# Kernel tuning notes

Measured on AMD Instinct MI355X. Metric: run time of the kernel, lower is better.

## Reference

```python
import jax, jax.numpy as jnp
import numpy as np
import math

B, T, C, NH, NLQ, NLKV, DHR = 2, 1024, 2048, 16, 512, 512, 64
HS = C // NH


def _rope(x, cos, sin):
    # x: [B,T,H,D]; cos/sin: [T,D//2]. Rotates pairs (even,odd) like torch apply_rotary_emb.
    xr = x.reshape(x.shape[:-1] + (-1, 2))
    re, im = xr[..., 0], xr[..., 1]
    c = cos[None, :, None, :]
    s = sin[None, :, None, :]
    out = jnp.stack([re * c - im * s, re * s + im * c], axis=-1)
    return out.reshape(x.shape)


def setup_inputs() -> dict:
    key = jax.random.key(0)
    ks = jax.random.split(key, 9)
    sc = jnp.float32(0.02)
    x = jax.random.normal(ks[0], (B, T, C), jnp.float32)
    W_dq = jax.random.normal(ks[1], (NLQ, C), jnp.float32) * sc
    W_uq = jax.random.normal(ks[2], (C, NLQ), jnp.float32) * sc
    W_dkv = jax.random.normal(ks[3], (NLKV, C), jnp.float32) * sc
    W_uk = jax.random.normal(ks[4], (C, NLKV), jnp.float32) * sc
    W_uv = jax.random.normal(ks[5], (C, NLKV), jnp.float32) * sc
    W_qr = jax.random.normal(ks[6], (NH * DHR, NLQ), jnp.float32) * sc
    W_kr = jax.random.normal(ks[7], (DHR, C), jnp.float32) * sc
    W_o = jax.random.normal(ks[8], (C, C), jnp.float32) * sc
    inv = 1.0 / (10000.0 ** (np.arange(0, DHR, 2, dtype=np.float64) / DHR))
    fr = np.outer(np.arange(T), inv)
    freqs_cos = jnp.asarray(np.cos(fr), jnp.float32)
    freqs_sin = jnp.asarray(np.sin(fr), jnp.float32)
    return {"x": x, "freqs_cos": freqs_cos, "freqs_sin": freqs_sin,
            "W_dq": W_dq, "W_uq": W_uq, "W_dkv": W_dkv, "W_uk": W_uk,
            "W_uv": W_uv, "W_qr": W_qr, "W_kr": W_kr, "W_o": W_o}


def reference(x, freqs_cos, freqs_sin, W_dq, W_uq, W_dkv, W_uk, W_uv, W_qr, W_kr, W_o):
    # Training path of FullMHLA (no kv_cache, dropout=0).
    # Absorbed matrices: same memory reinterpretation as torch .view on [out,in] weights.
    k_eff = jnp.einsum('qhd,hdk->hqk', W_uq.reshape(NLQ, NH, HS), W_uk.reshape(NH, HS, NLKV))  # [nh,nlq,nlkv]
    v_eff = (W_uv.T @ W_o.T).reshape(NLKV, NH, HS)  # used as [nlkv,nh,hs]

    c_q = x @ W_dq.T            # [B,T,nlq]
    c_kv = x @ W_dkv.T          # [B,T,nlkv]

    # content scores: c_q @ k_eff @ c_kv^T
    q_abs = jnp.einsum('btq,hqk->bhtk', c_q, k_eff)          # [B,nh,T,nlkv]
    attn_c = jnp.einsum('bhtk,bsk->bhts', q_abs, c_kv)       # [B,nh,T,T]

    # decoupled RoPE scores
    c_kr = x @ W_kr.T                                         # [B,T,dhr]
    k_r = _rope(c_kr[:, :, None, :], freqs_cos, freqs_sin)[:, :, 0, :]   # [B,T,dhr]
    c_qr = (c_q @ W_qr.T).reshape(B, T, NH, DHR)
    q_r = _rope(c_qr, freqs_cos, freqs_sin)                   # [B,T,nh,dhr]
    attn_r = jnp.einsum('bthd,bsd->bhts', q_r, k_r)           # [B,nh,T,T]

    attn = (attn_c + attn_r) / math.sqrt(HS + DHR)
    mask = jnp.triu(jnp.ones((T, T), dtype=bool), k=1)
    attn = jnp.where(mask[None, None], jnp.float32(-jnp.inf), attn)
    attn = jax.nn.softmax(attn, axis=-1)

    # y = attn @ c_kv @ v_eff
    lat = jnp.einsum('bhts,bsk->bhtk', attn, c_kv)            # [B,nh,T,nlkv]
    y = jnp.einsum('bhtk,khd->bthd', lat, v_eff)              # [B,T,nh,hs]
    return y.reshape(B, T, C)
```

## Files before the change

### kernel.cpp

```cpp
#include <hip/hip_runtime.h>

#define Bv   2
#define Tv   1024
#define Cv   2048
#define NHv  16

typedef unsigned short u16;
typedef __attribute__((ext_vector_type(8))) short bf8_t;
typedef __attribute__((ext_vector_type(4))) float f4_t;
typedef __attribute__((ext_vector_type(4))) unsigned short u16x4;
typedef __attribute__((ext_vector_type(8))) unsigned short u16x8;

__device__ __forceinline__ u16 f2bf(float f) {
  union { float f; unsigned u; } v; v.f = f;
  unsigned r = v.u + 0x7fffu + ((v.u >> 16) & 1u);
  return (u16)(r >> 16);
}
__device__ __forceinline__ float bf2f(u16 b) {
  return __uint_as_float((unsigned)b << 16);
}
__device__ __forceinline__ void glds16(const u16* gp, u16* lp) {
  __builtin_amdgcn_global_load_lds(
      (const __attribute__((address_space(1))) void*)gp,
      (__attribute__((address_space(3))) void*)lp, 16, 0, 0);
}

struct Job {
  const u16* A; const u16* B; void* C;
  long sA1, sA2, sB1, sB2, sC1, sC2;
  int K, lda, ldb, ldc, Nact, zdiv, ntx, nty, out_bf;
};
struct JobPack3 { Job j[3]; int cum[4]; };

__global__ __launch_bounds__(256) void gemm_multi(JobPack3 P) {
  const int bid = blockIdx.x;
  const int ji = (bid >= P.cum[1] ? 1 : 0) + (bid >= P.cum[2] ? 1 : 0);
  const Job& J = P.j[ji];
  int local = bid - P.cum[ji];
  const int x = local % J.ntx;
  int rest = local / J.ntx;
  const int y = rest % J.nty;
  const int z = rest / J.nty;
  const int m0 = y * 128, n0 = x * 128;

  const int z1 = z / J.zdiv, z2 = z % J.zdiv;
  const u16* A = J.A + z1 * J.sA1 + z2 * J.sA2;
  const u16* B = J.B + z1 * J.sB1 + z2 * J.sB2;
  const int K = J.K, lda = J.lda, ldb = J.ldb, ldc = J.ldc, Nact = J.Nact;

  __shared__ u16 SMEM[16384];
  u16* As = SMEM;
  u16* Bs = SMEM + 8192;

  const int tid = threadIdx.x, w = tid >> 6, ln = tid & 63;
  const int my = w >> 1, mx = w & 1;
  const int g = ln >> 4, m = ln & 15;

  f4_t acc[4][4];
#pragma unroll
  for (int i = 0; i < 4; ++i)
#pragma unroll
    for (int j = 0; j < 4; ++j) acc[i][j] = (f4_t)0.f;

  for (int k0 = 0; k0 < K; k0 += 64) {
#pragma unroll
    for (int q = 0; q < 4; ++q) {
      int r = 32 * w + 8 * q + (ln >> 3);
      int c = ((ln & 7) - r) & 7;
      glds16(&A[(long)(m0 + r) * lda + k0 + c * 8], &As[(32 * w + 8 * q) * 64]);
      glds16(&B[(long)(n0 + r) * ldb + k0 + c * 8], &Bs[(32 * w + 8 * q) * 64]);
    }
    __syncthreads();
#pragma unroll
    for (int kh = 0; kh < 2; ++kh) {
      bf8_t af[4], bg[4];
#pragma unroll
      for (int mt = 0; mt < 4; ++mt) {
        int row = my * 64 + mt * 16 + m;
        af[mt] = *(const bf8_t*)&As[row * 64 + (((kh * 4 + g) + row) & 7) * 8];
      }
#pragma unroll
      for (int nt = 0; nt < 4; ++nt) {
        int row = mx * 64 + nt * 16 + m;
        bg[nt] = *(const bf8_t*)&Bs[row * 64 + (((kh * 4 + g) + row) & 7) * 8];
      }
#pragma unroll
      for (int mt = 0; mt < 4; ++mt)
#pragma unroll
        for (int nt = 0; nt < 4; ++nt)
          acc[mt][nt] = __builtin_amdgcn_mfma_f32_16x16x32_bf16(
              af[mt], bg[nt], acc[mt][nt], 0, 0, 0);
    }
    __syncthreads();
  }

  if (J.out_bf) {
    u16* Es = SMEM + w * 4096;
#pragma unroll
    for (int mt = 0; mt < 4; ++mt)
#pragma unroll
      for (int nt = 0; nt < 4; ++nt)
#pragma unroll
        for (int r = 0; r < 4; ++r) {
          int row = mt * 16 + g * 4 + r;
          int col = nt * 16 + m;
          Es[row * 64 + (((col >> 3) + row) & 7) * 8 + (col & 7)] =
              f2bf(acc[mt][nt][r]);
        }
    __syncthreads();
    u16* C = (u16*)J.C + z1 * J.sC1 + z2 * J.sC2;
    const long rowbase = (long)(m0 + my * 64 + ln) * ldc + n0 + mx * 64;
#pragma unroll
    for (int c = 0; c < 8; ++c) {
      if (n0 + mx * 64 + c * 8 < Nact) {
        u16x8 v = *(const u16x8*)&Es[ln * 64 + ((c + ln) & 7) * 8];
        *(u16x8*)&C[rowbase + c * 8] = v;
      }
    }
  } else {
    float* C = (float*)J.C + z1 * J.sC1 + z2 * J.sC2;
#pragma unroll
    for (int mt = 0; mt < 4; ++mt)
#pragma unroll
      for (int nt = 0; nt < 4; ++nt)
#pragma unroll
        for (int r = 0; r < 4; ++r) {
          int row = m0 + my * 64 + mt * 16 + g * 4 + r;
          int col = n0 + mx * 64 + nt * 16 + m;
          if (col < Nact) C[(long)row * ldc + col] = acc[mt][nt][r];
        }
  }
}

__global__ __launch_bounds__(256, 3) void attn_part(
    const u16* __restrict__ Qcat,
    const u16* __restrict__ Kcat,
    const u16* __restrict__ ZT,
    float* __restrict__ Opart,
    float* __restrict__ ml,
    float* __restrict__ out) {
  const int x = blockIdx.x;
  const int bh = x & 31, item = x >> 5;
  const int b = bh >> 4, h = bh & 15;
  static const int qtab[40] = {2,3,4,5,6,6,7,7,8,8,9,9,10,10,10,11,11,11,
                               12,12,12,13,13,13,14,14,14,14,15,15,15,15,
                               0,1,4,5,8,9,12,13};
  static const int ctab[40] = {0,0,0,0,0,1,0,1,0,1,0,1,0,1,2,0,1,2,
                               0,1,2,0,1,2,0,1,2,3,0,1,2,3,
                               0,0,1,1,2,2,3,3};
  const int qt = qtab[item], ch = ctab[item];
  const int ns = (qt >> 1) + 1;
  const int s0t = 2 * ch, s1t = min(2 * ch + 2, ns);
  const bool full = (ch == 0) && (qt <= 3);

  __shared__ u16 As[4096];
  __shared__ u16 Bs[8192];
  __shared__ u16 Ps[8192];

  const int tid = threadIdx.x, w = tid >> 6, ln = tid & 63;
  const int g = ln >> 4, m = ln & 15;

  const u16* Qb = Qcat + (long)bh * 589824 + (long)qt * 64 * 576;
  const u16* Kb = Kcat + (long)b * 589824;
  const u16* Zb = ZT + (long)bh * 131072;

  f4_t O[8];
#pragma unroll
  for (int j = 0; j < 8; ++j) O[j] = (f4_t)0.f;
  float mrow[4], lrow[4];
#pragma unroll
  for (int r = 0; r < 4; ++r) { mrow[r] = -3e38f; lrow[r] = 0.f; }

  const float scale = 0.07216878364870322f;

  for (int st = s0t; st < s1t; ++st) {
    f4_t S[8];
#pragma unroll
    for (int j = 0; j < 8; ++j) S[j] = (f4_t)0.f;

    for (int k0 = 0; k0 < 576; k0 += 64) {
#pragma unroll
      for (int q = 0; q < 2; ++q) {
        int r = 16 * w + 8 * q + (ln >> 3);
        int c = ((ln & 7) - r) & 7;
        glds16(&Qb[(long)r * 576 + k0 + c * 8], &As[(16 * w + 8 * q) * 64]);
      }
#pragma unroll
      for (int q = 0; q < 4; ++q) {
        int r = 32 * w + 8 * q + (ln >> 3);
        int c = ((ln & 7) - r) & 7;
        glds16(&Kb[(long)(st * 128 + r) * 576 + k0 + c * 8],
               &Bs[(32 * w + 8 * q) * 64]);
      }
      __syncthreads();
#pragma unroll
      for (int kh = 0; kh < 2; ++kh) {
        int qrow = 16 * w + m;
        bf8_t af = *(const bf8_t*)&As[qrow * 64 + (((kh * 4 + g) + qrow) & 7) * 8];
#pragma unroll
        for (int nt = 0; nt < 8; ++nt) {
          int row = nt * 16 + m;
          bf8_t bb = *(const bf8_t*)&Bs[row * 64 + (((kh * 4 + g) + row) & 7) * 8];
          S[nt] = __builtin_amdgcn_mfma_f32_16x16x32_bf16(af, bb, S[nt], 0, 0, 0);
        }
      }
      __syncthreads();
    }

    const bool diag = (st == (qt >> 1));
#pragma unroll
    for (int nt = 0; nt < 8; ++nt)
#pragma unroll
      for (int r = 0; r < 4; ++r) {
        float v = S[nt][r] * scale;
        if (diag &&
            (st * 128 + nt * 16 + m) > (qt * 64 + 16 * w + g * 4 + r))
          v = -3e38f;
        S[nt][r] = v;
      }

#pragma unroll
    for (int r = 0; r < 4; ++r) {
      float mx = S[0][r];
#pragma unroll
      for (int nt = 1; nt < 8; ++nt) mx = fmaxf(mx, S[nt][r]);
#pragma unroll
      for (int o = 1; o < 16; o <<= 1) mx = fmaxf(mx, __shfl_xor(mx, o, 64));
      float mn = fmaxf(mrow[r], mx);
      float al = __expf(mrow[r] - mn);
      mrow[r] = mn;
      float rs = 0.f;
#pragma unroll
      for (int nt = 0; nt < 8; ++nt) {
        float p = __expf(S[nt][r] - mn);
        S[nt][r] = p;
        rs += p;
      }
#pragma unroll
      for (int o = 1; o < 16; o <<= 1) rs += __shfl_xor(rs, o, 64);
      lrow[r] = lrow[r] * al + rs;
#pragma unroll
      for (int nt = 0; nt < 8; ++nt) O[nt][r] *= al;
    }

#pragma unroll
    for (int nt = 0; nt < 8; ++nt) {
      int colc = nt * 2 + (m >> 3), cole = m & 7;
#pragma unroll
      for (int r = 0; r < 4; ++r) {
        int row = 16 * w + g * 4 + r;
        Ps[row * 128 + ((colc + row) & 15) * 8 + cole] = f2bf(S[nt][r]);
      }
    }

#pragma unroll
    for (int kb = 0; kb < 2; ++kb) {
      __syncthreads();
#pragma unroll
      for (int q = 0; q < 4; ++q) {
        int r = 32 * w + 8 * q + (ln >> 3);
        int c = ((ln & 7) - r) & 7;
        glds16(&Zb[(long)r * 1024 + st * 128 + kb * 64 + c * 8],
               &Bs[(32 * w + 8 * q) * 64]);
      }
      __syncthreads();
#pragma unroll
      for (int kh = 0; kh < 2; ++kh) {
        int qrow = 16 * w + m;
        int chk = kb * 8 + kh * 4 + g;
        bf8_t af = *(const bf8_t*)&Ps[qrow * 128 + ((chk + qrow) & 15) * 8];
#pragma unroll
        for (int nt = 0; nt < 8; ++nt) {
          int row = nt * 16 + m;
          bf8_t bb = *(const bf8_t*)&Bs[row * 64 + (((kh * 4 + g) + row) & 7) * 8];
          O[nt] = __builtin_amdgcn_mfma_f32_16x16x32_bf16(af, bb, O[nt], 0, 0, 0);
        }
      }
    }
    __syncthreads();
  }

  if (full) {
    float* ob = out + ((long)b * Tv + qt * 64 + 16 * w) * 2048 + h * 128;
#pragma unroll
    for (int r = 0; r < 4; ++r) {
      float inv = 1.0f / lrow[r];
#pragma unroll
      for (int nt = 0; nt < 8; ++nt)
        ob[(long)(g * 4 + r) * 2048 + nt * 16 + m] = O[nt][r] * inv;
    }
  } else {
    float* Ob = Opart + (long)x * 8192;
#pragma unroll
    for (int r = 0; r < 4; ++r) {
      int row = 16 * w + g * 4 + r;
#pragma unroll
      for (int nt = 0; nt < 8; ++nt)
        Ob[(long)row * 128 + nt * 16 + m] = O[nt][r];
      if (m == 0) {
        ml[(long)x * 128 + row] = mrow[r];
        ml[(long)x * 128 + 64 + row] = lrow[r];
      }
    }
  }
}

__global__ __launch_bounds__(256) void attn_merge(
    const float* __restrict__ Opart, const float* __restrict__ ml,
    float* __restrict__ out) {
  const int i = blockIdx.x;
  const int rg = i & 3;
  const int combo = i >> 2;
  const int bh = combo & 31, qt = 4 + (combo >> 5);
  const int b = bh >> 4, h = bh & 15;
  static const int NCH[16] = {1,1,1,1,2,2,2,2,3,3,3,3,4,4,4,4};
  static const int ITEM[64] = {
      32,0,0,0,  33,0,0,0,  0,0,0,0,   1,0,0,0,
      2,34,0,0,  3,35,0,0,  4,5,0,0,   6,7,0,0,
      8,9,36,0,  10,11,37,0, 12,13,14,0, 15,16,17,0,
      18,19,20,38, 21,22,23,39, 24,25,26,27, 28,29,30,31};
  const int nch = NCH[qt];
  const int r = threadIdx.x >> 5, c4 = threadIdx.x & 31;
  float* ob = out + ((long)b * Tv + qt * 64 + rg * 16) * 2048 + h * 128;
#pragma unroll
  for (int rr = 0; rr < 2; ++rr) {
    const int lrow = r + rr * 8;
    const int row = rg * 16 + lrow;
    float M = -3e38f, mi[4], li[4];
    for (int k = 0; k < nch; ++k) {
      long p = (long)ITEM[qt * 4 + k] * 32 + bh;
      mi[k] = ml[p * 128 + row];
      li[k] = ml[p * 128 + 64 + row];
      M = fmaxf(M, mi[k]);
    }
    float L = 0.f;
    float ax = 0.f, ay = 0.f, az = 0.f, aw = 0.f;
    for (int k = 0; k < nch; ++k) {
      long p = (long)ITEM[qt * 4 + k] * 32 + bh;
      float e = __expf(mi[k] - M);
      L += li[k] * e;
      float4 v = *(const float4*)&Opart[p * 8192 + (long)row * 128 + c4 * 4];
      ax += v.x * e; ay += v.y * e; az += v.z * e; aw += v.w * e;
    }
    const float inv = 1.0f / L;
    float4 o4 = {ax * inv, ay * inv, az * inv, aw * inv};
    *(float4*)&ob[(long)lrow * 2048 + c4 * 4] = o4;
  }
}

struct CastArgs {
  const float* src[6];
  u16* dst[6];
  long cum[7];
  const float* wkr;
  u16* w3;
};
__global__ void cast_all(CastArgs a, long total4) {
  long i = (long)blockIdx.x * 256 + threadIdx.x;
  if (i < total4) {
    int seg = 0;
    while (i >= a.cum[seg + 1]) ++seg;
    long j = i - a.cum[seg];
    float4 vv = ((const float4*)a.src[seg])[j];
    u16x4 o;
    o[0] = f2bf(vv.x); o[1] = f2bf(vv.y); o[2] = f2bf(vv.z); o[3] = f2bf(vv.w);
    ((u16x4*)a.dst[seg])[j] = o;
  } else {
    long j = i - total4;
    u16x4* W4 = (u16x4*)a.w3;
    if (j < 32768) {
      float4 vv = ((const float4*)a.wkr)[j];
      u16x4 o;
      o[0] = f2bf(vv.x); o[1] = f2bf(vv.y); o[2] = f2bf(vv.z); o[3] = f2bf(vv.w);
      W4[557056 + j] = o;
    } else if (j < 65536) {
      W4[262144 + (j - 32768)] = (u16x4)0;
    } else {
      W4[589824 + (j - 65536)] = (u16x4)0;
    }
  }
}

__global__ __launch_bounds__(256) void tcast2(const float* __restrict__ s0,
                                              u16* __restrict__ d0,
                                              const float* __restrict__ s1,
                                              u16* __restrict__ d1) {
  const float* in = blockIdx.z ? s1 : s0;
  u16* out = blockIdx.z ? d1 : d0;
  __shared__ u16 t[32][33];
  int c0 = blockIdx.x * 32, r0 = blockIdx.y * 32;
  int tx = threadIdx.x & 31, ty = threadIdx.x >> 5;
  for (int i = ty; i < 32; i += 8)
    t[i][tx] = f2bf(in[(long)(r0 + i) * 512 + c0 + tx]);
  __syncthreads();
  for (int i = ty; i < 32; i += 8)
    out[(long)(c0 + i) * 2048 + r0 + tx] = t[tx][i];
}

__global__ void rope_fused(u16* __restrict__ Kcat, const u16* __restrict__ cqr,
                           u16* __restrict__ Qcat,
                           const float* __restrict__ cosf,
                           const float* __restrict__ sinf) {
  int idx = blockIdx.x * 256 + threadIdx.x;
  if (idx < 65536) {
    int i = idx & 31, t = (idx >> 5) & 1023, b = idx >> 15;
    float c = cosf[t * 32 + i], s = sinf[t * 32 + i];
    u16* p = Kcat + ((long)(b * Tv + t) * 576 + 512 + 2 * i);
    float re = bf2f(p[0]), im = bf2f(p[1]);
    p[0] = f2bf(re * c - im * s);
    p[1] = f2bf(re * s + im * c);
  } else {
    int j = idx - 65536;
    int i = j & 31, h = (j >> 5) & 15, t = (j >> 9) & 1023, b = j >> 19;
    float c = cosf[t * 32 + i], s = sinf[t * 32 + i];
    const u16* src = cqr + ((long)(b * Tv + t) * 1024 + h * 64 + 2 * i);
    float re = bf2f(src[0]), im = bf2f(src[1]);
    u16* dst = Qcat + (((long)(b * NHv + h) * Tv + t) * 576 + 512 + 2 * i);
    dst[0] = f2bf(re * c - im * s);
    dst[1] = f2bf(re * s + im * c);
  }
}

__global__ void vred(const float* __restrict__ P, u16* __restrict__ veffT) {
  int i = blockIdx.x * 256 + threadIdx.x;
  float4 v0 = ((const float4*)P)[i];
  float4 v1 = ((const float4*)P)[262144 + i];
  float4 v2 = ((const float4*)P)[524288 + i];
  float4 v3 = ((const float4*)P)[786432 + i];
  u16x4 o;
  o[0] = f2bf(v0.x + v1.x + v2.x + v3.x);
  o[1] = f2bf(v0.y + v1.y + v2.y + v3.y);
  o[2] = f2bf(v0.z + v1.z + v2.z + v3.z);
  o[3] = f2bf(v0.w + v1.w + v2.w + v3.w);
  ((u16x4*)veffT)[i] = o;
}

extern "C" void kernel_launch(void* const* d_in, const int* in_sizes, int n_in,
                              void* d_out, int out_size, void* d_ws,
                              size_t ws_size, hipStream_t stream) {
  const float* x    = (const float*)d_in[0];
  const float* fcos = (const float*)d_in[1];
  const float* fsin = (const float*)d_in[2];
  const float* Wdq  = (const float*)d_in[3];
  const float* Wuq  = (const float*)d_in[4];
  const float* Wdkv = (const float*)d_in[5];
  const float* Wuk  = (const float*)d_in[6];
  const float* Wuv  = (const float*)d_in[7];
  const float* Wqr  = (const float*)d_in[8];
  const float* Wkr  = (const float*)d_in[9];
  const float* Wo   = (const float*)d_in[10];
  float* out = (float*)d_out;

  u16* ws = (u16*)d_ws;
  u16* cq     = ws;
  u16* Kcat   = cq + 1179648;
  u16* veffT  = Kcat + 1179648;
  u16* Qcat   = veffT + 1048576;
  u16* W3     = Qcat + 18874368;
  u16* x_bf   = W3 + 2490368;
  u16* Wqr_bf = x_bf + 4194304;
  u16* Wuq_bf = Wqr_bf + 524288;
  u16* Wo_bf  = Wuq_bf + 1048576;
  u16* WukT   = Wo_bf + 4194304;
  u16* WuvT   = WukT + 1048576;
  u16* cqr    = WuvT + 1048576;
  u16* keffT  = cqr + 2097152;
  u16* ZTbuf  = keffT + 4194304;
  float* Vprt  = (float*)(ZTbuf + 4194304);
  float* Opart = Vprt + 4194304;
  float* mlbuf = Opart + 10485760;

  {
    CastArgs a;
    a.src[0] = x;    a.dst[0] = x_bf;
    a.src[1] = Wdq;  a.dst[1] = W3;
    a.src[2] = Wdkv; a.dst[2] = W3 + 576 * 2048;
    a.src[3] = Wqr;  a.dst[3] = Wqr_bf;
    a.src[4] = Wuq;  a.dst[4] = Wuq_bf;
    a.src[5] = Wo;   a.dst[5] = Wo_bf;
    a.cum[0] = 0;        a.cum[1] = 1048576; a.cum[2] = 1310720;
    a.cum[3] = 1572864;  a.cum[4] = 1703936; a.cum[5] = 1966080;
    a.cum[6] = 3014656;
    a.wkr = Wkr; a.w3 = W3;
    cast_all<<<12160, 256, 0, stream>>>(a, 3014656L);
  }
  tcast2<<<dim3(16, 64, 2), 256, 0, stream>>>(Wuk, WukT, Wuv, WuvT);

  {
    JobPack3 P;
    P.j[0] = {x_bf, W3, cq, 0, 0, (long)576 * 2048, 0, 1179648, 0,
              2048, 2048, 2048, 576, 576, 1, 5, 16, 1};
    P.j[1] = {Wo_bf, WuvT, Vprt, 512, 0, 512, 0, 1048576, 0,
              512, 2048, 2048, 512, 512, 1, 4, 16, 0};
    P.j[2] = {WukT, Wuq_bf, keffT, 0, 128, 0, 128, 0, 262144,
              128, 2048, 2048, 512, 512, 16, 4, 4, 1};
    P.cum[0] = 0; P.cum[1] = 160; P.cum[2] = 416; P.cum[3] = 672;
    gemm_multi<<<672, 256, 0, stream>>>(P);
  }
  vred<<<1024, 256, 0, stream>>>(Vprt, veffT);

  {
    JobPack3 P;
    P.j[0] = {cq, keffT, Qcat, 589824, 0, 0, 262144, 9437184, 589824,
              512, 576, 512, 576, 512, 16, 4, 8, 1};
    P.j[1] = {veffT, Kcat, ZTbuf, 0, 65536, 589824, 0, 2097152, 131072,
              512, 512, 576, 1024, 1024, 16, 8, 1, 1};
    P.j[2] = {cq, Wqr_bf, cqr, 0, 0, 0, 0, 0, 0,
              512, 576, 512, 1024, 1024, 1, 8, 16, 1};
    P.cum[0] = 0; P.cum[1] = 1024; P.cum[2] = 1280; P.cum[3] = 1408;
    gemm_multi<<<1408, 256, 0, stream>>>(P);
  }

  rope_fused<<<4352, 256, 0, stream>>>(Kcat, cqr, Qcat, fcos, fsin);

  attn_part<<<1280, 256, 0, stream>>>(Qcat, Kcat, ZTbuf, Opart, mlbuf, out);
  attn_merge<<<1536, 256, 0, stream>>>(Opart, mlbuf, out);
}
```

Before: 287.6 us.

## Double-buffer K tiles in LDS and load Q fragments directly into registers

Splits the K staging buffer in the attention kernel into two LDS halves so the next K tile (or the first Z tile) is prefetched while MFMAs run on the current one. This removes one barrier per k-step. Q fragments now go straight from global memory into registers with their own double buffer, replacing the As LDS staging. The Z loads for the PV product are overlapped the same way, and s_setprio is raised around the MFMA blocks. In exchange, register pressure rises, and every k-step now issues uncoalesced per-lane global loads for Q.

```diff
diff --git a/kernel.cpp b/kernel.cpp
--- a/kernel.cpp
+++ b/kernel.cpp
@@ -153,8 +153,7 @@
   const int s0t = 2 * ch, s1t = min(2 * ch + 2, ns);
   const bool full = (ch == 0) && (qt <= 3);
 
-  __shared__ u16 As[4096];
-  __shared__ u16 Bs[8192];
+  __shared__ u16 Bs[2][8192];
   __shared__ u16 Ps[8192];
 
   const int tid = threadIdx.x, w = tid >> 6, ln = tid & 63;
@@ -164,6 +163,8 @@
   const u16* Kb = Kcat + (long)b * 589824;
   const u16* Zb = ZT + (long)bh * 131072;
 
+  const long qoff = (long)(16 * w + m) * 576;
+
   f4_t O[8];
 #pragma unroll
   for (int j = 0; j < 8; ++j) O[j] = (f4_t)0.f;
@@ -173,38 +174,63 @@
 
   const float scale = 0.07216878364870322f;
 
+  bf8_t qf[2][2];
+
   for (int st = s0t; st < s1t; ++st) {
     f4_t S[8];
 #pragma unroll
     for (int j = 0; j < 8; ++j) S[j] = (f4_t)0.f;
 
-    for (int k0 = 0; k0 < 576; k0 += 64) {
-#pragma unroll
-      for (int q = 0; q < 2; ++q) {
-        int r = 16 * w + 8 * q + (ln >> 3);
-        int c = ((ln & 7) - r) & 7;
-        glds16(&Qb[(long)r * 576 + k0 + c * 8], &As[(16 * w + 8 * q) * 64]);
-      }
-#pragma unroll
-      for (int q = 0; q < 4; ++q) {
-        int r = 32 * w + 8 * q + (ln >> 3);
-        int c = ((ln & 7) - r) & 7;
-        glds16(&Kb[(long)(st * 128 + r) * 576 + k0 + c * 8],
-               &Bs[(32 * w + 8 * q) * 64]);
-      }
-      __syncthreads();
+#pragma unroll
+    for (int q = 0; q < 4; ++q) {
+      int r = 32 * w + 8 * q + (ln >> 3);
+      int c = ((ln & 7) - r) & 7;
+      glds16(&Kb[(long)(st * 128 + r) * 576 + c * 8],
+             &Bs[1][(32 * w + 8 * q) * 64]);
+    }
+#pragma unroll
+    for (int kh = 0; kh < 2; ++kh)
+      qf[0][kh] = *(const bf8_t*)&Qb[qoff + kh * 32 + g * 8];
+    __syncthreads();
+
+#pragma unroll
+    for (int t = 0; t < 9; ++t) {
+      if (t < 8) {
+        const int k0 = (t + 1) * 64;
+#pragma unroll
+        for (int kh = 0; kh < 2; ++kh)
+          qf[(t + 1) & 1][kh] =
+              *(const bf8_t*)&Qb[qoff + k0 + kh * 32 + g * 8];
+#pragma unroll
+        for (int q = 0; q < 4; ++q) {
+          int r = 32 * w + 8 * q + (ln >> 3);
+          int c = ((ln & 7) - r) & 7;
+          glds16(&Kb[(long)(st * 128 + r) * 576 + k0 + c * 8],
+                 &Bs[t & 1][(32 * w + 8 * q) * 64]);
+        }
+      } else {
+#pragma unroll
+        for (int q = 0; q < 4; ++q) {
+          int r = 32 * w + 8 * q + (ln >> 3);
+          int c = ((ln & 7) - r) & 7;
+          glds16(&Zb[(long)r * 1024 + st * 128 + c * 8],
+                 &Bs[0][(32 * w + 8 * q) * 64]);
+        }
+      }
+      const u16* Bc = Bs[1 - (t & 1)];
+      __builtin_amdgcn_s_setprio(1);
 #pragma unroll
       for (int kh = 0; kh < 2; ++kh) {
-        int qrow = 16 * w + m;
-        bf8_t af = *(const bf8_t*)&As[qrow * 64 + (((kh * 4 + g) + qrow) & 7) * 8];
+        bf8_t af = qf[t & 1][kh];
 #pragma unroll
         for (int nt = 0; nt < 8; ++nt) {
           int row = nt * 16 + m;
-          bf8_t bb = *(const bf8_t*)&Bs[row * 64 + (((kh * 4 + g) + row) & 7) * 8];
+          bf8_t bb = *(const bf8_t*)&Bc[row * 64 + (((kh * 4 + g) + row) & 7) * 8];
           S[nt] = __builtin_amdgcn_mfma_f32_16x16x32_bf16(af, bb, S[nt], 0, 0, 0);
         }
       }
-      __syncthreads();
+      __builtin_amdgcn_s_setprio(0);
+      if (t < 8) __syncthreads();
     }
 
     const bool diag = (st == (qt >> 1));
@@ -252,31 +278,46 @@
         Ps[row * 128 + ((colc + row) & 15) * 8 + cole] = f2bf(S[nt][r]);
       }
     }
-
-#pragma unroll
-    for (int kb = 0; kb < 2; ++kb) {
-      __syncthreads();
-#pragma unroll
-      for (int q = 0; q < 4; ++q) {
-        int r = 32 * w + 8 * q + (ln >> 3);
-        int c = ((ln & 7) - r) & 7;
-        glds16(&Zb[(long)r * 1024 + st * 128 + kb * 64 + c * 8],
-               &Bs[(32 * w + 8 * q) * 64]);
-      }
-      __syncthreads();
-#pragma unroll
-      for (int kh = 0; kh < 2; ++kh) {
-        int qrow = 16 * w + m;
-        int chk = kb * 8 + kh * 4 + g;
-        bf8_t af = *(const bf8_t*)&Ps[qrow * 128 + ((chk + qrow) & 15) * 8];
-#pragma unroll
-        for (int nt = 0; nt < 8; ++nt) {
-          int row = nt * 16 + m;
-          bf8_t bb = *(const bf8_t*)&Bs[row * 64 + (((kh * 4 + g) + row) & 7) * 8];
-          O[nt] = __builtin_amdgcn_mfma_f32_16x16x32_bf16(af, bb, O[nt], 0, 0, 0);
-        }
-      }
-    }
+    __syncthreads();
+
+#pragma unroll
+    for (int q = 0; q < 4; ++q) {
+      int r = 32 * w + 8 * q + (ln >> 3);
+      int c = ((ln & 7) - r) & 7;
+      glds16(&Zb[(long)r * 1024 + st * 128 + 64 + c * 8],
+             &Bs[1][(32 * w + 8 * q) * 64]);
+    }
+
+    __builtin_amdgcn_s_setprio(1);
+#pragma unroll
+    for (int kh = 0; kh < 2; ++kh) {
+      int qrow = 16 * w + m;
+      int chk = kh * 4 + g;
+      bf8_t af = *(const bf8_t*)&Ps[qrow * 128 + ((chk + qrow) & 15) * 8];
+#pragma unroll
+      for (int nt = 0; nt < 8; ++nt) {
+        int row = nt * 16 + m;
+        bf8_t bb = *(const bf8_t*)&Bs[0][row * 64 + (((kh * 4 + g) + row) & 7) * 8];
+        O[nt] = __builtin_amdgcn_mfma_f32_16x16x32_bf16(af, bb, O[nt], 0, 0, 0);
+      }
+    }
+    __builtin_amdgcn_s_setprio(0);
+    __syncthreads();
+
+    __builtin_amdgcn_s_setprio(1);
+#pragma unroll
+    for (int kh = 0; kh < 2; ++kh) {
+      int qrow = 16 * w + m;
+      int chk = 8 + kh * 4 + g;
+      bf8_t af = *(const bf8_t*)&Ps[qrow * 128 + ((chk + qrow) & 15) * 8];
+#pragma unroll
+      for (int nt = 0; nt < 8; ++nt) {
+        int row = nt * 16 + m;
+        bf8_t bb = *(const bf8_t*)&Bs[1][row * 64 + (((kh * 4 + g) + row) & 7) * 8];
+        O[nt] = __builtin_amdgcn_mfma_f32_16x16x32_bf16(af, bb, O[nt], 0, 0, 0);
+      }
+    }
+    __builtin_amdgcn_s_setprio(0);
     __syncthreads();
   }
 
```

Measured after the change: 340.6 us. 18.4% more time.

## Reassociate query absorption: project through Wuq then Wuk instead of precomputed keff

Applied to the files above, without the earlier changes.

Replaces the precomputed absorbed matrix keff = Wuq·Wuk and the large cq·keff GEMM with two smaller GEMMs: cq·Wuq^T producing per-head queries, then a per-head multiply by Wuk into Qcat. This removes the keff GEMM and cuts the FLOPs of the query projection substantially. Wuq is now transposed in a generalized three-job transpose-cast kernel. It adds one extra kernel launch and an intermediate 2048-wide bf16 buffer round trip.

```diff
diff --git a/kernel.cpp b/kernel.cpp
--- a/kernel.cpp
+++ b/kernel.cpp
@@ -381,20 +381,24 @@
   }
 }
 
-__global__ __launch_bounds__(256) void tcast2(const float* __restrict__ s0,
-                                              u16* __restrict__ d0,
-                                              const float* __restrict__ s1,
-                                              u16* __restrict__ d1) {
-  const float* in = blockIdx.z ? s1 : s0;
-  u16* out = blockIdx.z ? d1 : d0;
-  __shared__ u16 t[32][33];
-  int c0 = blockIdx.x * 32, r0 = blockIdx.y * 32;
-  int tx = threadIdx.x & 31, ty = threadIdx.x >> 5;
+struct TcArgs { const float* s[3]; u16* d[3]; };
+__global__ __launch_bounds__(256) void tcastg(TcArgs a) {
+  const int bid = blockIdx.x;
+  const int job = bid >> 10, t = bid & 1023;
+  const float* in = a.s[job];
+  u16* out = a.d[job];
+  const int R = (job == 2) ? 512 : 2048;
+  const int C = (job == 2) ? 2048 : 512;
+  const int xt = (job == 2) ? 64 : 16;
+  const int x = t % xt, y = t / xt;
+  __shared__ u16 sm[32][33];
+  const int c0 = x * 32, r0 = y * 32;
+  const int tx = threadIdx.x & 31, ty = threadIdx.x >> 5;
   for (int i = ty; i < 32; i += 8)
-    t[i][tx] = f2bf(in[(long)(r0 + i) * 512 + c0 + tx]);
+    sm[i][tx] = f2bf(in[(long)(r0 + i) * C + c0 + tx]);
   __syncthreads();
   for (int i = ty; i < 32; i += 8)
-    out[(long)(c0 + i) * 2048 + r0 + tx] = t[tx][i];
+    out[(long)(c0 + i) * R + r0 + tx] = sm[tx][i];
 }
 
 __global__ void rope_fused(u16* __restrict__ Kcat, const u16* __restrict__ cqr,
@@ -459,13 +463,13 @@
   u16* W3     = Qcat + 18874368;
   u16* x_bf   = W3 + 2490368;
   u16* Wqr_bf = x_bf + 4194304;
-  u16* Wuq_bf = Wqr_bf + 524288;
-  u16* Wo_bf  = Wuq_bf + 1048576;
+  u16* WuqT   = Wqr_bf + 524288;
+  u16* Wo_bf  = WuqT + 1048576;
   u16* WukT   = Wo_bf + 4194304;
   u16* WuvT   = WukT + 1048576;
   u16* cqr    = WuvT + 1048576;
-  u16* keffT  = cqr + 2097152;
-  u16* ZTbuf  = keffT + 4194304;
+  u16* qup    = cqr + 2097152;
+  u16* ZTbuf  = qup + 4194304;
   float* Vprt  = (float*)(ZTbuf + 4194304);
   float* Opart = Vprt + 4194304;
   float* mlbuf = Opart + 10485760;
@@ -476,15 +480,21 @@
     a.src[1] = Wdq;  a.dst[1] = W3;
     a.src[2] = Wdkv; a.dst[2] = W3 + 576 * 2048;
     a.src[3] = Wqr;  a.dst[3] = Wqr_bf;
-    a.src[4] = Wuq;  a.dst[4] = Wuq_bf;
+    a.src[4] = Wo;   a.dst[4] = Wo_bf;
     a.src[5] = Wo;   a.dst[5] = Wo_bf;
     a.cum[0] = 0;        a.cum[1] = 1048576; a.cum[2] = 1310720;
-    a.cum[3] = 1572864;  a.cum[4] = 1703936; a.cum[5] = 1966080;
-    a.cum[6] = 3014656;
+    a.cum[3] = 1572864;  a.cum[4] = 1703936; a.cum[5] = 2752512;
+    a.cum[6] = 2752512;
     a.wkr = Wkr; a.w3 = W3;
-    cast_all<<<12160, 256, 0, stream>>>(a, 3014656L);
-  }
-  tcast2<<<dim3(16, 64, 2), 256, 0, stream>>>(Wuk, WukT, Wuv, WuvT);
+    cast_all<<<11136, 256, 0, stream>>>(a, 2752512L);
+  }
+  {
+    TcArgs t;
+    t.s[0] = Wuk; t.d[0] = WukT;
+    t.s[1] = Wuv; t.d[1] = WuvT;
+    t.s[2] = Wuq; t.d[2] = WuqT;
+    tcastg<<<3072, 256, 0, stream>>>(t);
+  }
 
   {
     JobPack3 P;
@@ -492,23 +502,32 @@
               2048, 2048, 2048, 576, 576, 1, 5, 16, 1};
     P.j[1] = {Wo_bf, WuvT, Vprt, 512, 0, 512, 0, 1048576, 0,
               512, 2048, 2048, 512, 512, 1, 4, 16, 0};
-    P.j[2] = {WukT, Wuq_bf, keffT, 0, 128, 0, 128, 0, 262144,
-              128, 2048, 2048, 512, 512, 16, 4, 4, 1};
-    P.cum[0] = 0; P.cum[1] = 160; P.cum[2] = 416; P.cum[3] = 672;
-    gemm_multi<<<672, 256, 0, stream>>>(P);
+    P.j[2] = P.j[1];
+    P.cum[0] = 0; P.cum[1] = 160; P.cum[2] = 416; P.cum[3] = 416;
+    gemm_multi<<<416, 256, 0, stream>>>(P);
   }
   vred<<<1024, 256, 0, stream>>>(Vprt, veffT);
 
   {
     JobPack3 P;
-    P.j[0] = {cq, keffT, Qcat, 589824, 0, 0, 262144, 9437184, 589824,
-              512, 576, 512, 576, 512, 16, 4, 8, 1};
+    P.j[0] = {cq, WuqT, qup, 0, 0, 0, 0, 0, 0,
+              512, 576, 512, 2048, 2048, 1, 16, 16, 1};
     P.j[1] = {veffT, Kcat, ZTbuf, 0, 65536, 589824, 0, 2097152, 131072,
               512, 512, 576, 1024, 1024, 16, 8, 1, 1};
     P.j[2] = {cq, Wqr_bf, cqr, 0, 0, 0, 0, 0, 0,
               512, 576, 512, 1024, 1024, 1, 8, 16, 1};
-    P.cum[0] = 0; P.cum[1] = 1024; P.cum[2] = 1280; P.cum[3] = 1408;
-    gemm_multi<<<1408, 256, 0, stream>>>(P);
+    P.cum[0] = 0; P.cum[1] = 256; P.cum[2] = 512; P.cum[3] = 640;
+    gemm_multi<<<640, 256, 0, stream>>>(P);
+  }
+
+  {
+    JobPack3 P;
+    P.j[0] = {qup, WukT, Qcat, 2097152, 128, 0, 128, 9437184, 589824,
+              128, 2048, 2048, 576, 512, 16, 4, 8, 1};
+    P.j[1] = P.j[0];
+    P.j[2] = P.j[0];
+    P.cum[0] = 0; P.cum[1] = 1024; P.cum[2] = 1024; P.cum[3] = 1024;
+    gemm_multi<<<1024, 256, 0, stream>>>(P);
   }
 
   rope_fused<<<4352, 256, 0, stream>>>(Kcat, cqr, Qcat, fcos, fsin);
```

Result: no change. 293.1 us (+1.9%).
